# Optimization experiments

Hardware: AMD Instinct MI355X
Metric: run time of the kernel (lower is better)

## Reference

```python
import jax, jax.numpy as jnp
from jax import lax
import numpy as np

DN = ('NCHW', 'OIHW', 'NCHW')

def _bn(x, g, b):
    # BatchNorm2d in training mode: batch statistics, biased variance, eps=1e-5
    m = jnp.mean(x, axis=(0, 2, 3), keepdims=True)
    v = jnp.var(x, axis=(0, 2, 3), keepdims=True)
    return g[None, :, None, None] * (x - m) * lax.rsqrt(v + 1e-5) + b[None, :, None, None]

def _conv(x, w, b, s, p):
    y = lax.conv_general_dilated(x, w, (s, s), [(p, p), (p, p)], dimension_numbers=DN)
    return y + b[None, :, None, None]

def _convt(x, w, b, s, p):
    # torch ConvTranspose2d weight layout [in, out, k, k]; equivalent to
    # input-dilated conv with flipped, transposed kernel and padding k-1-p.
    k = w.shape[2]
    pp = k - 1 - p
    w2 = jnp.flip(w, (2, 3)).transpose(1, 0, 2, 3)  # [out, in, k, k]
    y = lax.conv_general_dilated(x, w2, (1, 1), [(pp, pp), (pp, pp)],
                                 lhs_dilation=(s, s), dimension_numbers=DN)
    return y + b[None, :, None, None]

def setup_inputs() -> dict:
    key = jax.random.key(0)
    ks = jax.random.split(key, 16)
    f32 = jnp.float32
    def rn(i, shape, s):
        return jax.random.normal(ks[i], shape, f32) * s
    K = 256
    inp = {
        'x': jax.random.normal(ks[0], (128, 3, 64, 64), f32),
        'codebook': jax.random.uniform(ks[1], (256, 256), f32, -1.0 / K, 1.0 / K),
        'e_w1': rn(2, (64, 3, 3, 3), 0.19), 'e_b1': jnp.zeros((64,), f32),
        'e_g1': jnp.ones((64,), f32), 'e_be1': jnp.zeros((64,), f32),
        'e_w2': rn(3, (128, 64, 4, 4), 0.031), 'e_b2': jnp.zeros((128,), f32),
        'e_g2': jnp.ones((128,), f32), 'e_be2': jnp.zeros((128,), f32),
        'e_w3': rn(4, (192, 128, 4, 4), 0.022), 'e_b3': jnp.zeros((192,), f32),
        'e_g3': jnp.ones((192,), f32), 'e_be3': jnp.zeros((192,), f32),
        'e_w4': rn(5, (256, 192, 1, 1), 0.072), 'e_b4': jnp.zeros((256,), f32),
        'd_w1': rn(6, (256, 192, 1, 1), 0.062), 'd_b1': jnp.zeros((192,), f32),
        'd_g1': jnp.ones((192,), f32), 'd_be1': jnp.zeros((192,), f32),
        'd_w2': rn(7, (192, 128, 4, 4), 0.018), 'd_b2': jnp.zeros((128,), f32),
        'd_g2': jnp.ones((128,), f32), 'd_be2': jnp.zeros((128,), f32),
        'd_w3': rn(8, (128, 64, 4, 4), 0.022), 'd_b3': jnp.zeros((64,), f32),
        'd_g3': jnp.ones((64,), f32), 'd_be3': jnp.zeros((64,), f32),
        'd_w4': rn(9, (3, 64, 3, 3), 0.042), 'd_b4': jnp.zeros((3,), f32),
    }
    return inp

def reference(x, codebook,
              e_w1, e_b1, e_g1, e_be1, e_w2, e_b2, e_g2, e_be2,
              e_w3, e_b3, e_g3, e_be3, e_w4, e_b4,
              d_w1, d_b1, d_g1, d_be1, d_w2, d_b2, d_g2, d_be2,
              d_w3, d_b3, d_g3, d_be3, d_w4, d_b4):
    # encoder
    h = jax.nn.relu(_bn(_conv(x, e_w1, e_b1, 1, 1), e_g1, e_be1))
    h = jax.nn.relu(_bn(_conv(h, e_w2, e_b2, 2, 1), e_g2, e_be2))
    h = jax.nn.relu(_bn(_conv(h, e_w3, e_b3, 2, 1), e_g3, e_be3))
    h = _conv(h, e_w4, e_b4, 1, 0)  # [B, 256, 16, 16]
    B, C, H, W = h.shape
    Z = h.transpose(0, 2, 3, 1).reshape(-1, C)  # [N, D]
    # fused cdist via ||a||^2 + ||b||^2 - 2ab (argmin invariant to const offsets)
    d2 = (jnp.sum(Z * Z, axis=1, keepdims=True)
          + jnp.sum(codebook * codebook, axis=1)[None, :]
          - 2.0 * (Z @ codebook.T))  # [N, K]
    j = jnp.argmin(d2, axis=1)
    Wj = codebook[j]  # [N, D]
    loss_commit = jnp.mean(jnp.sum((Z - lax.stop_gradient(Wj)) ** 2, axis=1))
    loss_code = jnp.mean(jnp.sum((lax.stop_gradient(Z) - Wj) ** 2, axis=1))
    hq = Wj.reshape(B, H, W, C).transpose(0, 3, 1, 2)
    # decoder
    g = jax.nn.relu(_bn(_convt(hq, d_w1, d_b1, 1, 0), d_g1, d_be1))
    g = jax.nn.relu(_bn(_convt(g, d_w2, d_b2, 2, 1), d_g2, d_be2))
    g = jax.nn.relu(_bn(_convt(g, d_w3, d_b3, 2, 1), d_g3, d_be3))
    g = _conv(g, d_w4, d_b4, 1, 1)  # [B, 3, 64, 64]
    return g, loss_commit, loss_code
```

## Files before the change

kernel.cpp:

```cpp
#include <hip/hip_runtime.h>

#define TPB 256

typedef __attribute__((ext_vector_type(4))) float v4f;
typedef __attribute__((ext_vector_type(8))) short v8s;

__device__ __forceinline__ float us2f(unsigned int u) {
    union { unsigned int i; float f; } w; w.i = u << 16; return w.f;
}
__device__ __forceinline__ unsigned short f2us(float f) {
    union { float ff; unsigned int i; } w; w.ff = f;
    unsigned int u = w.i;
    return (unsigned short)((u + 0x7fffu + ((u >> 16) & 1u)) >> 16);
}
__device__ __forceinline__ void gl_lds16(const unsigned short* g, unsigned short* l) {
    __builtin_amdgcn_global_load_lds(
        (const __attribute__((address_space(1))) unsigned int*)g,
        (__attribute__((address_space(3))) unsigned int*)l, 16, 0, 0);
}

template<int CIN, int COUT, int KK>
__global__ __launch_bounds__(TPB) void repack_w(
    const float* __restrict__ w, unsigned short* __restrict__ o)
{
    int idx = blockIdx.x * TPB + threadIdx.x;
    if (idx >= KK * COUT * CIN) return;
    int ci = idx % CIN;
    int co = (idx / CIN) % COUT;
    int kk = idx / (CIN * COUT);
    o[idx] = f2us(w[((size_t)co * CIN + ci) * KK + kk]);
}
template<int CIN, int COUT>
__global__ __launch_bounds__(TPB) void repack_wt1(
    const float* __restrict__ w, unsigned short* __restrict__ o)
{
    int idx = blockIdx.x * TPB + threadIdx.x;
    if (idx >= CIN * COUT) return;
    int ci = idx % CIN;
    int co = idx / CIN;
    o[idx] = f2us(w[(size_t)ci * COUT + co]);
}
__global__ __launch_bounds__(TPB) void repack_we1(
    const float* __restrict__ w, unsigned short* __restrict__ o)
{
    int idx = blockIdx.x * TPB + threadIdx.x;
    if (idx >= 64 * 32) return;
    int k = idx & 31, co = idx >> 5;
    o[idx] = (k < 27) ? f2us(w[co * 27 + k]) : (unsigned short)0;
}
__global__ __launch_bounds__(TPB) void repack_wd4(
    const float* __restrict__ w, unsigned short* __restrict__ o)
{
    int idx = blockIdx.x * TPB + threadIdx.x;
    if (idx >= 18 * 512) return;
    int e = idx & 7;
    int lane = (idx >> 3) & 63;
    int kk = idx >> 9;
    int lr = lane & 15, lc = lane >> 4;
    int tap = kk >> 1, half = kk & 1;
    int ci = half * 32 + lc * 8 + e;
    o[idx] = (lr < 3) ? f2us(w[((size_t)lr * 64 + ci) * 9 + tap]) : (unsigned short)0;
}
template<int CIN, int COUT, int NCB>
__global__ __launch_bounds__(TPB) void repack_wct2(
    const float* __restrict__ w, unsigned short* __restrict__ o)
{
    constexpr int NCI = CIN / 64;
    int idx = blockIdx.x * TPB + threadIdx.x;
    if (idx >= 16 * COUT * CIN) return;
    int e = idx & 7;
    int lane = (idx >> 3) & 63;
    int seg8 = (idx >> 9) & 7;
    int u = idx >> 12;
    int cb = u % NCB;
    int u2 = u / NCB;
    int cc = u2 % NCI;
    int tk = u2 / NCI;
    int kidx = tk & 3, cls = tk >> 2;
    int lr = lane & 15, lc = lane >> 4;
    int kc = seg8 >> 2, sg = seg8 & 3;
    int co = cb * 64 + sg * 16 + lr;
    int ci = cc * 64 + kc * 32 + lc * 8 + e;
    int ohp = cls >> 1, owp = cls & 1;
    int kh = ((ohp + 1) & 1) + 2 * (kidx >> 1);
    int kw = ((owp + 1) & 1) + 2 * (kidx & 1);
    o[idx] = f2us(w[((size_t)ci * COUT + co) * 16 + kh * 4 + kw]);
}

__global__ __launch_bounds__(TPB) void im2col_e1(
    const float* __restrict__ x, unsigned short* __restrict__ A, int N)
{
    int p = blockIdx.x * TPB + threadIdx.x;
    int n = p >> 12, oh = (p >> 6) & 63, ow = p & 63;
    unsigned short row[32];
#pragma unroll
    for (int k = 0; k < 27; k++) {
        int ci = k / 9, tap = k % 9, kh = tap / 3, kw = tap % 3;
        int ih = oh - 1 + kh, iw = ow - 1 + kw;
        float v = ((unsigned)ih < 64u && (unsigned)iw < 64u)
            ? x[(((size_t)n * 3 + ci) * 64 + ih) * 64 + iw] : 0.f;
        row[k] = f2us(v);
    }
#pragma unroll
    for (int k = 27; k < 32; k++) row[k] = 0;
    int4* dst = (int4*)(A + (size_t)p * 32);
    const int4* src = (const int4*)row;
    dst[0] = src[0]; dst[1] = src[1]; dst[2] = src[2]; dst[3] = src[3];
}

__global__ __launch_bounds__(TPB) void e1_gemm(
    const unsigned short* __restrict__ A, const unsigned short* __restrict__ wrep,
    const float* __restrict__ bias, unsigned short* __restrict__ yout,
    float* __restrict__ part)
{
    __shared__ __align__(16) unsigned short Ab[8 * 512];
    __shared__ __align__(16) unsigned short Bb[4 * 512];

    const int t = threadIdx.x, lane = t & 63, wave = t >> 6;
    const int wm = wave >> 1, wn = wave & 1;
    const int m0 = (int)blockIdx.x * 128;
    const int lr = lane & 15, lc = lane >> 4;

    gl_lds16(A + (size_t)(m0 + wave * 16 + lr) * 32 + lc * 8, &Ab[wave * 512]);
    gl_lds16(A + (size_t)(m0 + (wave + 4) * 16 + lr) * 32 + lc * 8, &Ab[(wave + 4) * 512]);
    gl_lds16(wrep + (size_t)(wave * 16 + lr) * 32 + lc * 8, &Bb[wave * 512]);
    __syncthreads();

    v4f acc[4][2];
#pragma unroll
    for (int i = 0; i < 4; i++)
#pragma unroll
        for (int j = 0; j < 2; j++)
#pragma unroll
            for (int r = 0; r < 4; r++) acc[i][j][r] = 0.f;

    v8s a[4], b[2];
#pragma unroll
    for (int i = 0; i < 4; i++)
        a[i] = *(const v8s*)&Ab[(wm * 4 + i) * 512 + lane * 8];
#pragma unroll
    for (int j = 0; j < 2; j++)
        b[j] = *(const v8s*)&Bb[(wn * 2 + j) * 512 + lane * 8];
#pragma unroll
    for (int i = 0; i < 4; i++)
#pragma unroll
        for (int j = 0; j < 2; j++)
            acc[i][j] = __builtin_amdgcn_mfma_f32_16x16x32_bf16(a[i], b[j], acc[i][j], 0, 0, 0);

    float sloc[2], qloc[2];
#pragma unroll
    for (int j = 0; j < 2; j++) { sloc[j] = 0.f; qloc[j] = 0.f; }

#pragma unroll
    for (int i = 0; i < 4; i++) {
        int mr = wm * 64 + i * 16 + (lane >> 4) * 4;
#pragma unroll
        for (int j = 0; j < 2; j++) {
            int col = wn * 32 + j * 16 + (lane & 15);
            float bs = bias[col];
#pragma unroll
            for (int r = 0; r < 4; r++) {
                size_t g = (size_t)(m0 + mr + r) * 64 + col;
                float v = acc[i][j][r] + bs;
                yout[g] = f2us(v);
                sloc[j] += v;
                qloc[j] += v * v;
            }
        }
    }

    __syncthreads();
    float* red = (float*)Ab;
    for (int i = t; i < 128; i += TPB) red[i] = 0.f;
    __syncthreads();
#pragma unroll
    for (int j = 0; j < 2; j++) {
        float s = sloc[j], qv = qloc[j];
        s += __shfl_xor(s, 16); s += __shfl_xor(s, 32);
        qv += __shfl_xor(qv, 16); qv += __shfl_xor(qv, 32);
        if ((lane >> 4) == 0) {
            int cl = wn * 32 + j * 16 + (lane & 15);
            atomicAdd(&red[cl], s);
            atomicAdd(&red[64 + cl], qv);
        }
    }
    __syncthreads();
    int PB = (int)gridDim.x, pb = (int)blockIdx.x;
    for (int i = t; i < 64; i += TPB) {
        part[(size_t)i * PB + pb] = red[i];
        part[(size_t)(64 + i) * PB + pb] = red[64 + i];
    }
}

template<int CIN, int COUT, int HIN, int WIN, int K, int S, int P, int BN,
         int OUTM, int NYB>
__global__ __launch_bounds__(TPB) void conv_mfma(
    const unsigned short* __restrict__ xin, const unsigned short* __restrict__ wrep,
    const float* __restrict__ bias, void* __restrict__ yout, void* __restrict__ yout2,
    float* __restrict__ part, const unsigned short* __restrict__ zpage, int N)
{
    constexpr int HOUT = (HIN + 2 * P - K) / S + 1;
    constexpr int WOUT = (WIN + 2 * P - K) / S + 1;
    constexpr int RN = BN / 32;
    constexpr int BSEG = BN / 16;
    constexpr int NCI = CIN / 64;
    constexpr int NIT = K * K * NCI;
    __shared__ __align__(16) unsigned short Ab[2][16 * 512];
    __shared__ __align__(16) unsigned short Bb[2][2 * BSEG * 512];

    const int t = threadIdx.x, lane = t & 63, wave = t >> 6;
    const int wm = wave >> 1, wn = wave & 1;
    int m0, co0;
    if (NYB == 2) {
        int g = (int)blockIdx.x >> 3, xs = (int)blockIdx.x & 7;
        co0 = (g & 1) * BN;
        m0 = (((g >> 1) << 3) + xs) * 128;
    } else {
        m0 = (int)blockIdx.x * 128;
        co0 = 0;
    }
    const int lr = lane & 15, lc = lane >> 4;

    int n_[2], oh_[2], ow_[2];
#pragma unroll
    for (int i = 0; i < 2; i++) {
        int r = m0 + (wave + 4 * i) * 16 + lr;
        n_[i] = r / (HOUT * WOUT);
        int rem = r % (HOUT * WOUT);
        oh_[i] = rem / WOUT;
        ow_[i] = rem % WOUT;
    }

    v4f acc[4][RN];
#pragma unroll
    for (int i = 0; i < 4; i++)
#pragma unroll
        for (int j = 0; j < RN; j++)
#pragma unroll
            for (int r = 0; r < 4; r++) acc[i][j][r] = 0.f;

    auto do_stage = [&](int it, int pb) {
        const int kk = it / NCI;
        const int ci0 = (it % NCI) * 64;
        const int kh = kk / K, kw = kk % K;
#pragma unroll
        for (int i = 0; i < 2; i++) {
            int ih = oh_[i] * S - P + kh;
            int iw = ow_[i] * S - P + kw;
            bool av = (unsigned)ih < (unsigned)HIN && (unsigned)iw < (unsigned)WIN;
            const unsigned short* b0 = av
                ? xin + (((size_t)n_[i] * HIN + ih) * WIN + iw) * CIN + lc * 8 + ci0
                : zpage;
            gl_lds16(b0, &Ab[pb][(wave + 4 * i) * 512]);
            gl_lds16(av ? b0 + 32 : zpage, &Ab[pb][(8 + wave + 4 * i) * 512]);
        }
        const unsigned short* wt = wrep + (size_t)kk * COUT * CIN;
#pragma unroll
        for (int i = 0; i < 2; i++) {
            int sgb = wave + 4 * i;
            if (sgb < BSEG) {
                const unsigned short* wb =
                    wt + (size_t)(co0 + sgb * 16 + lr) * CIN + ci0 + lc * 8;
                gl_lds16(wb, &Bb[pb][sgb * 512]);
                gl_lds16(wb + 32, &Bb[pb][(BSEG + sgb) * 512]);
            }
        }
    };

    do_stage(0, 0);
    __syncthreads();

    for (int it = 0; it < NIT; ++it) {
        const int pb = it & 1;
        if (it + 1 < NIT) do_stage(it + 1, pb ^ 1);

#pragma unroll
        for (int kc = 0; kc < 2; kc++) {
            v8s a[4], b[RN];
#pragma unroll
            for (int i = 0; i < 4; i++)
                a[i] = *(const v8s*)&Ab[pb][(kc * 8 + wm * 4 + i) * 512 + lane * 8];
#pragma unroll
            for (int j = 0; j < RN; j++)
                b[j] = *(const v8s*)&Bb[pb][(kc * BSEG + wn * RN + j) * 512 + lane * 8];
#pragma unroll
            for (int i = 0; i < 4; i++)
#pragma unroll
                for (int j = 0; j < RN; j++)
                    acc[i][j] = __builtin_amdgcn_mfma_f32_16x16x32_bf16(a[i], b[j], acc[i][j], 0, 0, 0);
        }
        __syncthreads();
    }

    float sloc[RN], qloc[RN];
#pragma unroll
    for (int j = 0; j < RN; j++) { sloc[j] = 0.f; qloc[j] = 0.f; }

#pragma unroll
    for (int i = 0; i < 4; i++) {
        int mr = wm * 64 + i * 16 + (lane >> 4) * 4;
#pragma unroll
        for (int j = 0; j < RN; j++) {
            int col = co0 + wn * (BN / 2) + j * 16 + (lane & 15);
            float bs = bias[col];
#pragma unroll
            for (int r = 0; r < 4; r++) {
                size_t g = (size_t)(m0 + mr + r) * COUT + col;
                float v = acc[i][j][r] + bs;
                if (OUTM == 2) {
                    unsigned short h = f2us(v);
                    ((unsigned short*)yout)[g] = h;
                    ((unsigned short*)yout2)[g] = f2us(v - us2f(h));
                } else {
                    ((unsigned short*)yout)[g] = f2us(v);
                    sloc[j] += v;
                    qloc[j] += v * v;
                }
            }
        }
    }

    if (OUTM == 0) {
        __syncthreads();
        float* red = (float*)Ab;
        for (int i = t; i < 2 * BN; i += TPB) red[i] = 0.f;
        __syncthreads();
#pragma unroll
        for (int j = 0; j < RN; j++) {
            float s = sloc[j], qv = qloc[j];
            s += __shfl_xor(s, 16); s += __shfl_xor(s, 32);
            qv += __shfl_xor(qv, 16); qv += __shfl_xor(qv, 32);
            if ((lane >> 4) == 0) {
                int cl = wn * (BN / 2) + j * 16 + (lane & 15);
                atomicAdd(&red[cl], s);
                atomicAdd(&red[BN + cl], qv);
            }
        }
        __syncthreads();
        int pb = (NYB == 2) ? (m0 >> 7) : (int)blockIdx.x;
        int PB = (NYB == 2) ? ((int)gridDim.x >> 1) : (int)gridDim.x;
        for (int i = t; i < BN; i += TPB) {
            int col = co0 + i;
            part[(size_t)col * PB + pb] = red[i];
            part[(size_t)(COUT + col) * PB + pb] = red[BN + i];
        }
    }
}

template<int CIN, int COUT, int HIN, int WIN, int NCB, int IN_CLS>
__global__ __launch_bounds__(TPB) void convt_c(
    const unsigned short* __restrict__ xin, const unsigned short* __restrict__ wrep,
    const float* __restrict__ bias, unsigned short* __restrict__ yout,
    float* __restrict__ part, const unsigned short* __restrict__ zpage, int N)
{
    constexpr int NCI = CIN / 64;
    constexpr int NIT = 4 * NCI;
    __shared__ __align__(16) unsigned short Ab[2][16 * 1024];
    __shared__ __align__(16) unsigned short Bb[2][8 * 512];

    const int t = threadIdx.x, lane = t & 63, wave = t >> 6;
    int gdec = (int)blockIdx.x >> 3, xs = (int)blockIdx.x & 7;
    int cb = 0;
    if (NCB == 2) { cb = gdec & 1; gdec >>= 1; }
    const int cls = gdec & 3;
    const int tile = ((gdec >> 2) << 3) + xs;
    const int m0 = tile * 256;
    const int co0 = cb * 64;
    const int ohp = cls >> 1, owp = cls & 1;
    const int khb = (ohp + 1) & 1, kwb = (owp + 1) & 1;
    const int dh0 = (ohp + 1 - khb) >> 1, dw0 = (owp + 1 - kwb) >> 1;
    const int lr = lane & 15, lc = lane >> 4;

    const int jr7 = lane >> 3;
    const int sw = ((lane & 7) ^ jr7) * 8;

    int n_[4], i_[4], j0_[4];
#pragma unroll
    for (int q = 0; q < 4; q++) {
        int r0 = m0 + (wave * 4 + q) * 16;
        n_[q] = r0 / (HIN * WIN);
        int rem = r0 % (HIN * WIN);
        i_[q] = rem / WIN;
        j0_[q] = rem % WIN;
    }

    v4f acc[4][4];
#pragma unroll
    for (int i = 0; i < 4; i++)
#pragma unroll
        for (int j = 0; j < 4; j++)
#pragma unroll
            for (int r = 0; r < 4; r++) acc[i][j][r] = 0.f;

    auto stage = [&](int it, int buf) {
        const int tap = it / NCI, cc = it % NCI;
        const int dh = dh0 - (tap >> 1);
        const int dw = dw0 - (tap & 1);
#pragma unroll
        for (int q = 0; q < 4; q++) {
            const int ih = i_[q] + dh;
            const bool ihv = (unsigned)ih < (unsigned)HIN;
#pragma unroll
            for (int h = 0; h < 2; h++) {
                int iw = j0_[q] + h * 8 + jr7 + dw;
                bool av = ihv && (unsigned)iw < (unsigned)WIN;
                size_t ab;
                if (IN_CLS) {
                    int clsi = ((ih & 1) << 1) | (iw & 1);
                    ab = ((((size_t)clsi * N + n_[q]) * (HIN / 2) + (ih >> 1)) * (WIN / 2)
                         + (iw >> 1)) * CIN;
                } else {
                    ab = (((size_t)n_[q] * HIN + ih) * WIN + iw) * CIN;
                }
                const unsigned short* src = av ? xin + ab + cc * 64 + sw : zpage;
                gl_lds16(src, &Ab[buf][(wave * 4 + q) * 1024 + h * 512]);
            }
        }
        const unsigned short* wb = wrep
            + ((size_t)((cls * 4 + tap) * NCI + cc) * NCB + cb) * 4096;
        gl_lds16(wb + wave * 512 + lane * 8, &Bb[buf][wave * 512]);
        gl_lds16(wb + (4 + wave) * 512 + lane * 8, &Bb[buf][(4 + wave) * 512]);
    };

    auto compute = [&](int it, int buf) {
#pragma unroll
        for (int kc = 0; kc < 2; kc++) {
            v8s a[4], b[4];
#pragma unroll
            for (int i = 0; i < 4; i++)
                a[i] = *(const v8s*)&Ab[buf][(wave * 4 + i) * 1024 + lr * 64
                        + ((kc * 32 + lc * 8) ^ ((lr & 7) << 3))];
#pragma unroll
            for (int j = 0; j < 4; j++)
                b[j] = *(const v8s*)&Bb[buf][(kc * 4 + j) * 512 + lane * 8];
#pragma unroll
            for (int i = 0; i < 4; i++)
#pragma unroll
                for (int j = 0; j < 4; j++)
                    acc[i][j] = __builtin_amdgcn_mfma_f32_16x16x32_bf16(a[i], b[j], acc[i][j], 0, 0, 0);
        }
    };

    stage(0, 0);
    __syncthreads();

#pragma unroll
    for (int it = 0; it < NIT; ++it) {
        const int buf = it & 1;
        if (it + 1 < NIT) stage(it + 1, buf ^ 1);
        compute(it, buf);
        __syncthreads();
    }

    float sloc[4], qloc[4];
#pragma unroll
    for (int j = 0; j < 4; j++) { sloc[j] = 0.f; qloc[j] = 0.f; }

    const size_t clsbase = (size_t)cls * N * HIN * WIN;
#pragma unroll
    for (int i = 0; i < 4; i++) {
        int mr = wave * 64 + i * 16 + (lane >> 4) * 4;
#pragma unroll
        for (int j = 0; j < 4; j++) {
            int col = co0 + j * 16 + (lane & 15);
            float bs = bias[col];
#pragma unroll
            for (int r = 0; r < 4; r++) {
                size_t gi = (clsbase + m0 + mr + r) * COUT + col;
                float v = acc[i][j][r] + bs;
                yout[gi] = f2us(v);
                sloc[j] += v;
                qloc[j] += v * v;
            }
        }
    }

    float* red = (float*)Ab;
    for (int i = t; i < 128; i += TPB) red[i] = 0.f;
    __syncthreads();
#pragma unroll
    for (int j = 0; j < 4; j++) {
        float s = sloc[j], qv = qloc[j];
        s += __shfl_xor(s, 16); s += __shfl_xor(s, 32);
        qv += __shfl_xor(qv, 16); qv += __shfl_xor(qv, 32);
        if ((lane >> 4) == 0) {
            int cl = j * 16 + (lane & 15);
            atomicAdd(&red[cl], s);
            atomicAdd(&red[64 + cl], qv);
        }
    }
    __syncthreads();
    const int TILES = (N * HIN * WIN) >> 8;
    const int PB = 4 * TILES;
    const int pb = cls * TILES + tile;
    for (int i = t; i < 64; i += TPB) {
        part[(size_t)(co0 + i) * PB + pb] = red[i];
        part[(size_t)(COUT + co0 + i) * PB + pb] = red[64 + i];
    }
}

template<int C>
__global__ __launch_bounds__(64) void bn_reduce2(
    const float* __restrict__ part, float* __restrict__ st, int B)
{
    int i = blockIdx.x;
    int lane = threadIdx.x;
    float s = 0.f;
    for (int b = lane; b < B; b += 64) s += part[(size_t)i * B + b];
#pragma unroll
    for (int off = 1; off < 64; off <<= 1) s += __shfl_xor(s, off);
    if (lane == 0) st[i] = s;
}

template<int C>
__global__ __launch_bounds__(TPB) void bn_apply_v(
    unsigned short* __restrict__ x, const float* __restrict__ st,
    const float* __restrict__ g, const float* __restrict__ be, int M)
{
    __shared__ float sc[C], sh[C];
    int t = threadIdx.x;
    float cnt = (float)M;
    for (int c = t; c < C; c += TPB) {
        float m = st[c] / cnt;
        float v = st[C + c] / cnt - m * m;
        float s = g[c] * rsqrtf(v + 1e-5f);
        sc[c] = s;
        sh[c] = be[c] - m * s;
    }
    __syncthreads();
    constexpr int GPT = C / 8;
    size_t tot = (size_t)M * GPT;
    for (size_t slot = (size_t)blockIdx.x * TPB + t; slot < tot;
         slot += (size_t)gridDim.x * TPB) {
        int c0 = (int)(slot % GPT) * 8;
        int4 v = *(int4*)(x + slot * 8);
        unsigned int* vu = (unsigned int*)&v;
#pragma unroll
        for (int k = 0; k < 4; k++) {
            float f0 = fmaxf(us2f(vu[k] & 0xffffu) * sc[c0 + 2 * k] + sh[c0 + 2 * k], 0.f);
            float f1 = fmaxf(us2f(vu[k] >> 16) * sc[c0 + 2 * k + 1] + sh[c0 + 2 * k + 1], 0.f);
            vu[k] = (unsigned int)f2us(f0) | ((unsigned int)f2us(f1) << 16);
        }
        *(int4*)(x + slot * 8) = v;
    }
}

__global__ __launch_bounds__(TPB) void cb_prep(
    const float* __restrict__ cb, unsigned short* __restrict__ chb,
    unsigned short* __restrict__ clb, float* __restrict__ cn2)
{
    int j = blockIdx.x, d = threadIdx.x;
    float v = cb[j * 256 + d];
    unsigned short h = f2us(v);
    chb[j * 256 + d] = h;
    clb[j * 256 + d] = f2us(v - us2f(h));
    float s = v * v;
#pragma unroll
    for (int off = 1; off < 64; off <<= 1) s += __shfl_xor(s, off);
    __shared__ float p[4];
    if ((d & 63) == 0) p[d >> 6] = s;
    __syncthreads();
    if (d == 0) cn2[j] = p[0] + p[1] + p[2] + p[3];
}

__global__ __launch_bounds__(TPB) void vq_gemm(
    const unsigned short* __restrict__ zh, const unsigned short* __restrict__ zl,
    const unsigned short* __restrict__ chb, const unsigned short* __restrict__ clb,
    const float* __restrict__ cn2, float* __restrict__ valp, int* __restrict__ idxp)
{
    __shared__ __align__(16) unsigned short Ah[2][8 * 512];
    __shared__ __align__(16) unsigned short Al[2][8 * 512];
    __shared__ __align__(16) unsigned short Bh[2][8 * 512];
    __shared__ __align__(16) unsigned short Bl[2][8 * 512];

    const int t = threadIdx.x, lane = t & 63, wave = t >> 6;
    const int wm = wave >> 1, wn = wave & 1;
    const int gdec = (int)blockIdx.x >> 3, xs = (int)blockIdx.x & 7;
    const int cbk = gdec & 1;
    const int m0 = (((gdec >> 1) << 3) + xs) * 128;
    const int co0 = cbk * 128;
    const int lr = lane & 15, lc = lane >> 4;

    size_t a0 = (size_t)(m0 + wave * 16 + lr) * 256 + lc * 8;
    size_t a1 = a0 + 64 * 256;
    size_t b0 = (size_t)(co0 + wave * 16 + lr) * 256 + lc * 8;
    size_t b1 = b0 + 64 * 256;

    v4f acc[4][4];
#pragma unroll
    for (int i = 0; i < 4; i++)
#pragma unroll
        for (int j = 0; j < 4; j++)
#pragma unroll
            for (int r = 0; r < 4; r++) acc[i][j][r] = 0.f;

    auto do_stage = [&](int ci0, int pb) {
        gl_lds16(zh + a0 + ci0, &Ah[pb][wave * 512]);
        gl_lds16(zh + a1 + ci0, &Ah[pb][(wave + 4) * 512]);
        gl_lds16(zl + a0 + ci0, &Al[pb][wave * 512]);
        gl_lds16(zl + a1 + ci0, &Al[pb][(wave + 4) * 512]);
        gl_lds16(chb + b0 + ci0, &Bh[pb][wave * 512]);
        gl_lds16(chb + b1 + ci0, &Bh[pb][(wave + 4) * 512]);
        gl_lds16(clb + b0 + ci0, &Bl[pb][wave * 512]);
        gl_lds16(clb + b1 + ci0, &Bl[pb][(wave + 4) * 512]);
    };

    do_stage(0, 0);
    __syncthreads();

    for (int s = 0; s < 8; ++s) {
        const int pb = s & 1;
        if (s < 7) do_stage((s + 1) * 32, pb ^ 1);

        v8s a_h[4], a_l[4], b_h[4], b_l[4];
#pragma unroll
        for (int i = 0; i < 4; i++) {
            a_h[i] = *(const v8s*)&Ah[pb][(wm * 4 + i) * 512 + lane * 8];
            a_l[i] = *(const v8s*)&Al[pb][(wm * 4 + i) * 512 + lane * 8];
        }
#pragma unroll
        for (int j = 0; j < 4; j++) {
            b_h[j] = *(const v8s*)&Bh[pb][(wn * 4 + j) * 512 + lane * 8];
            b_l[j] = *(const v8s*)&Bl[pb][(wn * 4 + j) * 512 + lane * 8];
        }
#pragma unroll
        for (int i = 0; i < 4; i++)
#pragma unroll
            for (int j = 0; j < 4; j++) {
                acc[i][j] = __builtin_amdgcn_mfma_f32_16x16x32_bf16(a_h[i], b_h[j], acc[i][j], 0, 0, 0);
                acc[i][j] = __builtin_amdgcn_mfma_f32_16x16x32_bf16(a_h[i], b_l[j], acc[i][j], 0, 0, 0);
                acc[i][j] = __builtin_amdgcn_mfma_f32_16x16x32_bf16(a_l[i], b_h[j], acc[i][j], 0, 0, 0);
            }
        __syncthreads();
    }

#pragma unroll
    for (int i = 0; i < 4; i++) {
#pragma unroll
        for (int r = 0; r < 4; r++) {
            float best = 3.4e38f;
            int bi = 0;
#pragma unroll
            for (int j = 0; j < 4; j++) {
                int col = co0 + wn * 64 + j * 16 + (lane & 15);
                float d = cn2[col] - 2.f * acc[i][j][r];
                if (d < best || (d == best && col < bi)) { best = d; bi = col; }
            }
#pragma unroll
            for (int off = 1; off < 16; off <<= 1) {
                float ov = __shfl_xor(best, off);
                int oi = __shfl_xor(bi, off);
                if (ov < best || (ov == best && oi < bi)) { best = ov; bi = oi; }
            }
            if ((lane & 15) == 0) {
                int row = m0 + wm * 64 + i * 16 + (lane >> 4) * 4 + r;
                valp[(size_t)row * 4 + cbk * 2 + wn] = best;
                idxp[(size_t)row * 4 + cbk * 2 + wn] = bi;
            }
        }
    }
}

__global__ __launch_bounds__(TPB) void vq_gather2(
    const unsigned short* __restrict__ zh, const unsigned short* __restrict__ zl,
    const float* __restrict__ cb, const float* __restrict__ valp,
    const int* __restrict__ idxp, unsigned short* __restrict__ hq,
    float* __restrict__ rowloss)
{
    int row = blockIdx.x * 4 + (threadIdx.x >> 6);
    int lane = threadIdx.x & 63;
    float best = valp[(size_t)row * 4];
    int j = idxp[(size_t)row * 4];
#pragma unroll
    for (int c = 1; c < 4; c++) {
        float v = valp[(size_t)row * 4 + c];
        if (v < best) { best = v; j = idxp[(size_t)row * 4 + c]; }
    }
    ushort4 hv = *(const ushort4*)(zh + (size_t)row * 256 + lane * 4);
    ushort4 lv = *(const ushort4*)(zl + (size_t)row * 256 + lane * 4);
    float4 cv = *(const float4*)(cb + (size_t)j * 256 + lane * 4);
    float z0 = us2f(hv.x) + us2f(lv.x);
    float z1 = us2f(hv.y) + us2f(lv.y);
    float z2 = us2f(hv.z) + us2f(lv.z);
    float z3 = us2f(hv.w) + us2f(lv.w);
    float d0 = z0 - cv.x, d1 = z1 - cv.y, d2 = z2 - cv.z, d3 = z3 - cv.w;
    float d = d0 * d0 + d1 * d1 + d2 * d2 + d3 * d3;
#pragma unroll
    for (int off = 1; off < 64; off <<= 1) d += __shfl_xor(d, off);
    if (lane == 0) rowloss[row] = d;
    ushort4 o;
    o.x = f2us(cv.x); o.y = f2us(cv.y); o.z = f2us(cv.z); o.w = f2us(cv.w);
    *(ushort4*)(hq + (size_t)row * 256 + lane * 4) = o;
}

__global__ __launch_bounds__(TPB) void loss_reduce1(
    const float* __restrict__ rowloss, float* __restrict__ part64)
{
    int t = threadIdx.x;
    int base = blockIdx.x * 512 + t;
    float v = rowloss[base] + rowloss[base + 256];
#pragma unroll
    for (int off = 1; off < 64; off <<= 1) v += __shfl_xor(v, off);
    __shared__ float p[4];
    if ((t & 63) == 0) p[t >> 6] = v;
    __syncthreads();
    if (t == 0) part64[blockIdx.x] = p[0] + p[1] + p[2] + p[3];
}

__global__ __launch_bounds__(64) void loss_finalize(
    const float* __restrict__ part64, float* __restrict__ out2)
{
    float v = part64[threadIdx.x];
    for (int off = 32; off > 0; off >>= 1) v += __shfl_down(v, off);
    if (threadIdx.x == 0) {
        float m = v * (1.0f / 32768.0f);
        out2[0] = m;
        out2[1] = m;
    }
}

__global__ __launch_bounds__(TPB) void conv_d4(
    const unsigned short* __restrict__ xb, const unsigned short* __restrict__ wrep,
    const float* __restrict__ bias, float* __restrict__ out, int N)
{
    __shared__ __align__(16) unsigned short xsm[8 * 409 * 8];
    int4* xsI = (int4*)xsm;
    const int t = threadIdx.x;
    const int lane = t & 63, wave = t >> 6;
    const int lr = lane & 15, lc = lane >> 4;

    const int n = blockIdx.x >> 4;
    const int tile = blockIdx.x & 15;
    const int th = tile >> 2, tw = tile & 3;
    const int ihh0 = 8 * th - 1, iwh0 = 8 * tw - 1;

    for (int s = t; s < 3200; s += TPB) {
        int cls = s / 800;
        int rem = s % 800;
        int ihh_l = rem / 80;
        int i4 = rem % 80;
        int iwh_l = i4 >> 3, c8 = i4 & 7;
        int ihh_g = ihh0 + ihh_l;
        int iwh_g = iwh0 + iwh_l;
        int4 v;
        if ((unsigned)ihh_g < 32u && (unsigned)iwh_g < 32u) {
            size_t row = (((size_t)cls * 128 + n) * 32 + ihh_g) * 32 + iwh_g;
            v = *(const int4*)(xb + row * 64 + c8 * 8);
        } else {
            v.x = v.y = v.z = v.w = 0;
        }
        xsI[c8 * 409 + cls * 102 + ihh_l * 10 + iwh_l] = v;
    }
    __syncthreads();

    int abase[4][9];
#pragma unroll
    for (int q = 0; q < 4; q++) {
        int seg = wave * 4 + q;
        int oh = th * 16 + seg;
        int ow = tw * 16 + lr;
#pragma unroll
        for (int tap = 0; tap < 9; tap++) {
            int kh = tap / 3, kw = tap % 3;
            int ih = oh - 1 + kh, iw = ow - 1 + kw;
            int clsi = ((ih & 1) << 1) | (iw & 1);
            abase[q][tap] = clsi * 102 + ((ih >> 1) - ihh0) * 10 + ((iw >> 1) - iwh0);
        }
    }

    v4f acc[4];
#pragma unroll
    for (int q = 0; q < 4; q++)
#pragma unroll
        for (int r = 0; r < 4; r++) acc[q][r] = 0.f;

#pragma unroll
    for (int kk = 0; kk < 18; kk++) {
        const int tap = kk >> 1, half = kk & 1;
        const int c8 = half * 4 + lc;
        v8s b = *(const v8s*)(wrep + kk * 512 + lane * 8);
#pragma unroll
        for (int q = 0; q < 4; q++) {
            v8s a = *(const v8s*)&xsI[c8 * 409 + abase[q][tap]];
            acc[q] = __builtin_amdgcn_mfma_f32_16x16x32_bf16(a, b, acc[q], 0, 0, 0);
        }
    }

    if (lr < 3) {
        float bs = bias[lr];
#pragma unroll
        for (int q = 0; q < 4; q++) {
            int seg = wave * 4 + q;
            int oh = th * 16 + seg;
            int ow0 = tw * 16 + lc * 4;
            float4 v;
            v.x = acc[q][0] + bs; v.y = acc[q][1] + bs;
            v.z = acc[q][2] + bs; v.w = acc[q][3] + bs;
            *(float4*)&out[((size_t)n * 3 + lr) * 4096 + oh * 64 + ow0] = v;
        }
    }
}


extern "C" void kernel_launch(void* const* d_in, const int* in_sizes, int n_in,
                              void* d_out, int out_size, void* d_ws, size_t ws_size,
                              hipStream_t stream) {
    const float* x    = (const float*)d_in[0];
    const float* cb   = (const float*)d_in[1];
    const float* e_w1 = (const float*)d_in[2];  const float* e_b1 = (const float*)d_in[3];
    const float* e_g1 = (const float*)d_in[4];  const float* e_be1 = (const float*)d_in[5];
    const float* e_w2 = (const float*)d_in[6];  const float* e_b2 = (const float*)d_in[7];
    const float* e_g2 = (const float*)d_in[8];  const float* e_be2 = (const float*)d_in[9];
    const float* e_w3 = (const float*)d_in[10]; const float* e_b3 = (const float*)d_in[11];
    const float* e_g3 = (const float*)d_in[12]; const float* e_be3 = (const float*)d_in[13];
    const float* e_w4 = (const float*)d_in[14]; const float* e_b4 = (const float*)d_in[15];
    const float* d_w1 = (const float*)d_in[16]; const float* d_b1 = (const float*)d_in[17];
    const float* d_g1 = (const float*)d_in[18]; const float* d_be1 = (const float*)d_in[19];
    const float* d_w2 = (const float*)d_in[20]; const float* d_b2 = (const float*)d_in[21];
    const float* d_g2 = (const float*)d_in[22]; const float* d_be2 = (const float*)d_in[23];
    const float* d_w3 = (const float*)d_in[24]; const float* d_b3 = (const float*)d_in[25];
    const float* d_g3 = (const float*)d_in[26]; const float* d_be3 = (const float*)d_in[27];
    const float* d_w4 = (const float*)d_in[28]; const float* d_b4 = (const float*)d_in[29];

    float* ws = (float*)d_ws;
    unsigned short* h1 = (unsigned short*)(ws);
    unsigned short* g3 = h1;
    unsigned short* h2 = (unsigned short*)(ws + 16777216);
    unsigned short* g2 = h2;
    unsigned short* h3 = (unsigned short*)(ws + 25165824);
    unsigned short* g1 = h3;
    unsigned short* zh = (unsigned short*)(ws + 28311552);
    unsigned short* zl = (unsigned short*)(ws + 32505856);
    unsigned short* aim = zh;
    unsigned short* hq = (unsigned short*)(ws + 36700160);
    float* stats = ws + 40960000;
    unsigned short* we1 = (unsigned short*)(ws + 40963072);
    unsigned short* wd4r = (unsigned short*)(ws + 40964096);
    float* cn2 = ws + 40995904;
    unsigned short* chb = (unsigned short*)(ws + 40996160);
    unsigned short* clb = (unsigned short*)(ws + 41028928);
    unsigned short* wrep = (unsigned short*)(ws + 41061696);
    unsigned short* we2 = wrep + 0;
    unsigned short* we3 = wrep + 131072;
    unsigned short* we4 = wrep + 524288;
    unsigned short* wd1 = wrep + 573440;
    unsigned short* wd2 = wrep + 622592;
    unsigned short* wd3 = wrep + 1015808;
    float* part = ws + 41635136;
    float* valp = part;
    int* idxp = (int*)(part + 131072);
    float* rowloss = ws + 50023744;
    float* part64 = ws + 50122048;
    unsigned short* zpage = (unsigned short*)(ws + 50122112);
    float* out = (float*)d_out;
    float* losses = out + 1572864;

    const int N = 128;

    hipMemsetAsync(zpage, 0, 256, stream);

    repack_we1<<<8, TPB, 0, stream>>>(e_w1, we1);
    repack_wd4<<<36, TPB, 0, stream>>>(d_w4, wd4r);
    repack_w<64, 128, 16><<<512, TPB, 0, stream>>>(e_w2, we2);
    repack_w<128, 192, 16><<<1536, TPB, 0, stream>>>(e_w3, we3);
    repack_w<192, 256, 1><<<192, TPB, 0, stream>>>(e_w4, we4);
    repack_wt1<256, 192><<<192, TPB, 0, stream>>>(d_w1, wd1);
    repack_wct2<192, 128, 2><<<1536, TPB, 0, stream>>>(d_w2, wd2);
    repack_wct2<128, 64, 1><<<512, TPB, 0, stream>>>(d_w3, wd3);
    cb_prep<<<256, TPB, 0, stream>>>(cb, chb, clb, cn2);

    im2col_e1<<<2048, TPB, 0, stream>>>(x, aim, N);
    e1_gemm<<<4096, TPB, 0, stream>>>(aim, we1, e_b1, h1, part);
    bn_reduce2<64><<<128, 64, 0, stream>>>(part, stats + 0 * 512, 4096);
    bn_apply_v<64><<<4096, TPB, 0, stream>>>(h1, stats + 0 * 512, e_g1, e_be1, 524288);

    conv_mfma<64, 128, 64, 64, 4, 2, 1, 128, 0, 1>
        <<<1024, TPB, 0, stream>>>(h1, we2, e_b2, h2, nullptr, part, zpage, N);
    bn_reduce2<128><<<256, 64, 0, stream>>>(part, stats + 1 * 512, 1024);
    bn_apply_v<128><<<2048, TPB, 0, stream>>>(h2, stats + 1 * 512, e_g2, e_be2, 131072);

    conv_mfma<128, 192, 32, 32, 4, 2, 1, 96, 0, 2>
        <<<512, TPB, 0, stream>>>(h2, we3, e_b3, h3, nullptr, part, zpage, N);
    bn_reduce2<192><<<384, 64, 0, stream>>>(part, stats + 2 * 512, 256);
    bn_apply_v<192><<<1024, TPB, 0, stream>>>(h3, stats + 2 * 512, e_g3, e_be3, 32768);

    conv_mfma<192, 256, 16, 16, 1, 1, 0, 128, 2, 2>
        <<<512, TPB, 0, stream>>>(h3, we4, e_b4, zh, zl, nullptr, zpage, N);

    vq_gemm<<<512, TPB, 0, stream>>>(zh, zl, chb, clb, cn2, valp, idxp);
    vq_gather2<<<8192, TPB, 0, stream>>>(zh, zl, cb, valp, idxp, hq, rowloss);
    loss_reduce1<<<64, TPB, 0, stream>>>(rowloss, part64);
    loss_finalize<<<1, 64, 0, stream>>>(part64, losses);

    conv_mfma<256, 192, 16, 16, 1, 1, 0, 96, 0, 2>
        <<<512, TPB, 0, stream>>>(hq, wd1, d_b1, g1, nullptr, part, zpage, N);
    bn_reduce2<192><<<384, 64, 0, stream>>>(part, stats + 3 * 512, 256);
    bn_apply_v<192><<<1024, TPB, 0, stream>>>(g1, stats + 3 * 512, d_g1, d_be1, 32768);

    convt_c<192, 128, 16, 16, 2, 0>
        <<<1024, TPB, 0, stream>>>(g1, wd2, d_b2, g2, part, zpage, N);
    bn_reduce2<128><<<256, 64, 0, stream>>>(part, stats + 4 * 512, 512);
    bn_apply_v<128><<<2048, TPB, 0, stream>>>(g2, stats + 4 * 512, d_g2, d_be2, 131072);

    convt_c<128, 64, 32, 32, 1, 1>
        <<<2048, TPB, 0, stream>>>(g2, wd3, d_b3, g3, part, zpage, N);
    bn_reduce2<64><<<128, 64, 0, stream>>>(part, stats + 5 * 512, 2048);
    bn_apply_v<64><<<4096, TPB, 0, stream>>>(g3, stats + 5 * 512, d_g3, d_be3, 524288);

    conv_d4<<<2048, TPB, 0, stream>>>(g3, wd4r, d_b4, out, N);
}
```

Before: 603.8 us.

## Store e1 output in parity-class layout and add specialized stride-2 conv kernel

The first encoder GEMM now writes its output split into four spatial-parity classes (even/odd row and column), so each tap of the following 4x4 stride-2 conv reads a contiguous downsampled plane. A new conv_c kernel uses 256-row by 64-channel tiles with a double-buffered LDS pipeline, XOR-swizzled A reads and a new weight repack. It replaces the generic conv_mfma for the second encoder conv and changes the partial-stat count for the BN reduction. The scattered output writes in e1_gemm may coalesce less well.

After: 666.9 us (median of 2 runs). 1.1x slower.

```diff
diff --git a/kernel.cpp b/kernel.cpp
--- a/kernel.cpp
+++ b/kernel.cpp
@@ -60,6 +60,24 @@
     int tap = kk >> 1, half = kk & 1;
     int ci = half * 32 + lc * 8 + e;
     o[idx] = (lr < 3) ? f2us(w[((size_t)lr * 64 + ci) * 9 + tap]) : (unsigned short)0;
+}
+template<int CIN, int COUT, int NCB>
+__global__ __launch_bounds__(TPB) void repack_wf2(
+    const float* __restrict__ w, unsigned short* __restrict__ o)
+{
+    int idx = blockIdx.x * TPB + threadIdx.x;
+    if (idx >= 16 * COUT * CIN) return;
+    int e = idx & 7;
+    int lane = (idx >> 3) & 63;
+    int seg8 = (idx >> 9) & 7;
+    int u = idx >> 12;
+    int cb = u % NCB;
+    int tap = u / NCB;
+    int lr = lane & 15, lc = lane >> 4;
+    int kc = seg8 >> 2, sg = seg8 & 3;
+    int co = cb * 64 + sg * 16 + lr;
+    int ci = kc * 32 + lc * 8 + e;
+    o[idx] = f2us(w[((size_t)co * CIN + ci) * 16 + tap]);
 }
 template<int CIN, int COUT, int NCB>
 __global__ __launch_bounds__(TPB) void repack_wct2(
@@ -111,7 +129,7 @@
 __global__ __launch_bounds__(TPB) void e1_gemm(
     const unsigned short* __restrict__ A, const unsigned short* __restrict__ wrep,
     const float* __restrict__ bias, unsigned short* __restrict__ yout,
-    float* __restrict__ part)
+    float* __restrict__ part, int N)
 {
     __shared__ __align__(16) unsigned short Ab[8 * 512];
     __shared__ __align__(16) unsigned short Bb[4 * 512];
@@ -160,9 +178,12 @@
             float bs = bias[col];
 #pragma unroll
             for (int r = 0; r < 4; r++) {
-                size_t g = (size_t)(m0 + mr + r) * 64 + col;
+                int row = m0 + mr + r;
+                int n = row >> 12, oh = (row >> 6) & 63, ow = row & 63;
+                int cls = ((oh & 1) << 1) | (ow & 1);
+                size_t crow = ((((size_t)cls * N + n) * 32 + (oh >> 1)) * 32 + (ow >> 1));
                 float v = acc[i][j][r] + bs;
-                yout[g] = f2us(v);
+                yout[crow * 64 + col] = f2us(v);
                 sloc[j] += v;
                 qloc[j] += v * v;
             }
@@ -189,6 +210,147 @@
     for (int i = t; i < 64; i += TPB) {
         part[(size_t)i * PB + pb] = red[i];
         part[(size_t)(64 + i) * PB + pb] = red[64 + i];
+    }
+}
+
+template<int CIN, int COUT, int HO, int WO, int NCB>
+__global__ __launch_bounds__(TPB) void conv_c(
+    const unsigned short* __restrict__ xin, const unsigned short* __restrict__ wrep,
+    const float* __restrict__ bias, unsigned short* __restrict__ yout,
+    float* __restrict__ part, const unsigned short* __restrict__ zpage, int N)
+{
+    constexpr int NCI = CIN / 64;
+    constexpr int NIT = 16 * NCI;
+    __shared__ __align__(16) unsigned short Ab[2][16 * 1024];
+    __shared__ __align__(16) unsigned short Bb[2][8 * 512];
+
+    const int t = threadIdx.x, lane = t & 63, wave = t >> 6;
+    int gdec = (int)blockIdx.x >> 3, xs = (int)blockIdx.x & 7;
+    int cb = 0;
+    if (NCB >= 2) { cb = gdec % NCB; gdec /= NCB; }
+    const int tile = (gdec << 3) + xs;
+    const int m0 = tile * 256;
+    const int co0 = cb * 64;
+    const int lr = lane & 15, lc = lane >> 4;
+
+    const int jr7 = lane >> 3;
+    const int sw = ((lane & 7) ^ jr7) * 8;
+
+    int n_[4], oh_[4], ow0_[4];
+#pragma unroll
+    for (int q = 0; q < 4; q++) {
+        int r0 = m0 + (wave * 4 + q) * 16;
+        n_[q] = r0 / (HO * WO);
+        int rem = r0 % (HO * WO);
+        oh_[q] = rem / WO;
+        ow0_[q] = rem % WO;
+    }
+
+    v4f acc[4][4];
+#pragma unroll
+    for (int i = 0; i < 4; i++)
+#pragma unroll
+        for (int j = 0; j < 4; j++)
+#pragma unroll
+            for (int r = 0; r < 4; r++) acc[i][j][r] = 0.f;
+
+    auto stage = [&](int it, int buf) {
+        const int tap = it / NCI, cc = it % NCI;
+        const int kh = tap >> 2, kw = tap & 3;
+        const int dcls = (((kh + 1) & 1) << 1) | ((kw + 1) & 1);
+        const int dh2 = (kh - 1) >> 1;
+        const int dw2 = (kw - 1) >> 1;
+#pragma unroll
+        for (int q = 0; q < 4; q++) {
+            const int ih2 = oh_[q] + dh2;
+            const bool ihv = (unsigned)ih2 < (unsigned)HO;
+#pragma unroll
+            for (int h = 0; h < 2; h++) {
+                int iw2 = ow0_[q] + h * 8 + jr7 + dw2;
+                bool av = ihv && (unsigned)iw2 < (unsigned)WO;
+                size_t ab = ((((size_t)dcls * N + n_[q]) * HO + ih2) * WO + iw2) * CIN;
+                const unsigned short* src = av ? xin + ab + cc * 64 + sw : zpage;
+                gl_lds16(src, &Ab[buf][(wave * 4 + q) * 1024 + h * 512]);
+            }
+        }
+        const unsigned short* wb = wrep
+            + ((size_t)(tap * NCI + cc) * NCB + cb) * 4096;
+        gl_lds16(wb + wave * 512 + lane * 8, &Bb[buf][wave * 512]);
+        gl_lds16(wb + (4 + wave) * 512 + lane * 8, &Bb[buf][(4 + wave) * 512]);
+    };
+
+    auto compute = [&](int it, int buf) {
+#pragma unroll
+        for (int kc = 0; kc < 2; kc++) {
+            v8s a[4], b[4];
+#pragma unroll
+            for (int i = 0; i < 4; i++)
+                a[i] = *(const v8s*)&Ab[buf][(wave * 4 + i) * 1024 + lr * 64
+                        + ((kc * 32 + lc * 8) ^ ((lr & 7) << 3))];
+#pragma unroll
+            for (int j = 0; j < 4; j++)
+                b[j] = *(const v8s*)&Bb[buf][(kc * 4 + j) * 512 + lane * 8];
+#pragma unroll
+            for (int i = 0; i < 4; i++)
+#pragma unroll
+                for (int j = 0; j < 4; j++)
+                    acc[i][j] = __builtin_amdgcn_mfma_f32_16x16x32_bf16(a[i], b[j], acc[i][j], 0, 0, 0);
+        }
+    };
+
+    stage(0, 0);
+    __syncthreads();
+
+#pragma unroll
+    for (int it = 0; it < NIT; ++it) {
+        const int buf = it & 1;
+        if (it + 1 < NIT) stage(it + 1, buf ^ 1);
+        compute(it, buf);
+        __syncthreads();
+    }
+
+    float sloc[4], qloc[4];
+#pragma unroll
+    for (int j = 0; j < 4; j++) { sloc[j] = 0.f; qloc[j] = 0.f; }
+
+#pragma unroll
+    for (int i = 0; i < 4; i++) {
+        int mr = wave * 64 + i * 16 + (lane >> 4) * 4;
+#pragma unroll
+        for (int j = 0; j < 4; j++) {
+            int col = co0 + j * 16 + (lane & 15);
+            float bs = bias[col];
+#pragma unroll
+            for (int r = 0; r < 4; r++) {
+                size_t gi = (size_t)(m0 + mr + r) * COUT + col;
+                float v = acc[i][j][r] + bs;
+                yout[gi] = f2us(v);
+                sloc[j] += v;
+                qloc[j] += v * v;
+            }
+        }
+    }
+
+    float* red = (float*)Ab;
+    for (int i = t; i < 128; i += TPB) red[i] = 0.f;
+    __syncthreads();
+#pragma unroll
+    for (int j = 0; j < 4; j++) {
+        float s = sloc[j], qv = qloc[j];
+        s += __shfl_xor(s, 16); s += __shfl_xor(s, 32);
+        qv += __shfl_xor(qv, 16); qv += __shfl_xor(qv, 32);
+        if ((lane >> 4) == 0) {
+            int cl = j * 16 + (lane & 15);
+            atomicAdd(&red[cl], s);
+            atomicAdd(&red[64 + cl], qv);
+        }
+    }
+    __syncthreads();
+    const int TILES = (N * HO * WO) >> 8;
+    const int pb = tile;
+    for (int i = t; i < 64; i += TPB) {
+        part[(size_t)(co0 + i) * TILES + pb] = red[i];
+        part[(size_t)(COUT + co0 + i) * TILES + pb] = red[64 + i];
     }
 }
 
@@ -861,7 +1023,7 @@
 
     repack_we1<<<8, TPB, 0, stream>>>(e_w1, we1);
     repack_wd4<<<36, TPB, 0, stream>>>(d_w4, wd4r);
-    repack_w<64, 128, 16><<<512, TPB, 0, stream>>>(e_w2, we2);
+    repack_wf2<64, 128, 2><<<512, TPB, 0, stream>>>(e_w2, we2);
     repack_w<128, 192, 16><<<1536, TPB, 0, stream>>>(e_w3, we3);
     repack_w<192, 256, 1><<<192, TPB, 0, stream>>>(e_w4, we4);
     repack_wt1<256, 192><<<192, TPB, 0, stream>>>(d_w1, wd1);
@@ -870,13 +1032,13 @@
     cb_prep<<<256, TPB, 0, stream>>>(cb, chb, clb, cn2);
 
     im2col_e1<<<2048, TPB, 0, stream>>>(x, aim, N);
-    e1_gemm<<<4096, TPB, 0, stream>>>(aim, we1, e_b1, h1, part);
+    e1_gemm<<<4096, TPB, 0, stream>>>(aim, we1, e_b1, h1, part, N);
     bn_reduce2<64><<<128, 64, 0, stream>>>(part, stats + 0 * 512, 4096);
     bn_apply_v<64><<<4096, TPB, 0, stream>>>(h1, stats + 0 * 512, e_g1, e_be1, 524288);
 
-    conv_mfma<64, 128, 64, 64, 4, 2, 1, 128, 0, 1>
-        <<<1024, TPB, 0, stream>>>(h1, we2, e_b2, h2, nullptr, part, zpage, N);
-    bn_reduce2<128><<<256, 64, 0, stream>>>(part, stats + 1 * 512, 1024);
+    conv_c<64, 128, 32, 32, 2>
+        <<<1024, TPB, 0, stream>>>(h1, we2, e_b2, h2, part, zpage, N);
+    bn_reduce2<128><<<256, 64, 0, stream>>>(part, stats + 1 * 512, 512);
     bn_apply_v<128><<<2048, TPB, 0, stream>>>(h2, stats + 1 * 512, e_g2, e_be2, 131072);
 
     conv_mfma<128, 192, 32, 32, 4, 2, 1, 96, 0, 2>
```
